# Performance work log

Measured on AMD Instinct MI355X. Metric: run time of the kernel, lower is better.

The kernel has to match this reference:

```python
import jax, jax.numpy as jnp
import numpy as np
import math

D = 128      # out_dim (= d)
H = 4        # n_heads
DK = D // H  # d_k = 32
M = 5        # fixed num types in forward
NN = 15      # fixed N in forward
SQRT_DK = math.sqrt(DK)


def setup_inputs() -> dict:
    key = jax.random.key(0)
    ks = jax.random.split(key, 18)
    b, n = 1024, 64
    inp = {
        "node_inp": jax.random.normal(ks[0], (D, b, n), jnp.float32),
        "WW": jax.random.normal(ks[1], (b, M, n, NN), jnp.float32) * 0.1,
        "mask_matrix": jax.random.uniform(ks[2], (M * NN, n), jnp.float32),
        "R": jax.random.normal(ks[3], (b, H, n, n), jnp.float32),
        "attn_mask": jax.random.uniform(ks[4], (1, 1, n, 4 * n), jnp.float32),
        # learned parameters (xavier-ish scale)
        "WK": jax.random.normal(ks[5], (M, D, D), jnp.float32) * 0.05,
        "bK": jax.random.normal(ks[6], (M, D, 1), jnp.float32) * 0.05,
        "WQ": jax.random.normal(ks[7], (M, D, D), jnp.float32) * 0.05,
        "bQ": jax.random.normal(ks[8], (M, D, 1), jnp.float32) * 0.05,
        "WM": jax.random.normal(ks[9], (M, D, D), jnp.float32) * 0.05,
        "bM": jax.random.normal(ks[10], (M, D, 1), jnp.float32) * 0.05,
        "WB": jax.random.normal(ks[11], (M, D, D), jnp.float32) * 0.05,
        "bB": jax.random.normal(ks[12], (M, D, 1), jnp.float32) * 0.05,
        "Wmsgup": jax.random.normal(ks[13], (DK, DK), jnp.float32) * 0.1,
        "Wmsgdown": jax.random.normal(ks[14], (DK, DK), jnp.float32) * 0.1,
        "Wmsgleft": jax.random.normal(ks[15], (DK, DK), jnp.float32) * 0.1,
        "Wmsgright": jax.random.normal(ks[16], (DK, DK), jnp.float32) * 0.1,
    }
    return inp


def reference(node_inp, WW, mask_matrix, R, attn_mask,
              WK, bK, WQ, bQ, WM, bM, WB, bB,
              Wmsgup, Wmsgdown, Wmsgleft, Wmsgright):
    d, b, n = node_inp.shape
    # project node features through per-type mixing: (b, m, d, N)
    node_inp_m = jnp.einsum('dbn,bmnN->bmdN', node_inp, WW)

    def proj_perm(W, bias):
        # per-type linear then permute(0,2,1,3) before flatten (as K/Q do)
        x = jnp.einsum('mde,bmeN->bmdN', W, node_inp_m) + bias[None]  # (b,m,d,N)
        x = x.transpose(0, 2, 1, 3).reshape(b, d, M * NN)
        return x @ mask_matrix  # (b, d, n)

    K = proj_perm(WK, bK).reshape(b, H, DK, n)
    Q = proj_perm(WQ, bQ).reshape(b, H, DK, n)

    # message: NOTE original reshapes (b*m,d,N) -> (b,d,m*N) WITHOUT the permute; replicate faithfully
    msg = jnp.einsum('mde,bmeN->bmdN', WM, node_inp_m) + bM[None]  # (b,m,d,N)
    message = msg.reshape(b, d, M * NN) @ mask_matrix               # (b, d, n)

    A = jnp.einsum('bhki,bhkj->bhij', Q, K) / SQRT_DK               # (b,h,n,n)
    aw = jax.nn.softmax(R + A, axis=3)
    aw = jnp.where(jnp.isnan(aw), jnp.zeros_like(aw), aw)
    aw = jnp.tile(aw, (1, 1, 1, 4)) * attn_mask                     # (b,h,n,4n)

    res_msg = message.reshape(b, H, DK, n)
    Wmsg = jnp.concatenate([Wmsgup, Wmsgdown, Wmsgleft, Wmsgright], axis=1)  # (dk, 4dk)
    res = jnp.einsum('kq,bhkn->bhqn', Wmsg, res_msg)                # (b,h,4dk,n)
    res = res.reshape(b, H, DK, 4 * n)                               # faithful reshape

    B = jnp.einsum('bhnm,bhkm->bhkn', aw, res).reshape(b, d, n)
    B = jax.nn.gelu(B, approximate=False)

    Bm = jnp.einsum('bdn,bmnN->bmdN', B, WW)
    Bm = jnp.einsum('mde,bmeN->bmdN', WB, Bm) + bB[None]
    Bm = Bm.transpose(0, 2, 1, 3).reshape(b, d, M * NN) @ mask_matrix  # (b,d,n)
    out = Bm.transpose(1, 0, 2) + node_inp                             # (d,b,n)
    return (out, aw[0, 0])
```

## Files before the change

### kernel.cpp

```cpp
#include <hip/hip_runtime.h>
#include <math.h>

#define Dd 128
#define Hh 4
#define DKk 32
#define Mm 5
#define NNn 15
#define Bb 1024
#define Nn 64
#define MN 75
#define BN 65536
#define RSQRT_DK 0.17677669529663687f

typedef __attribute__((ext_vector_type(8))) short bf16x8;
typedef __attribute__((ext_vector_type(4))) float f32x4;

__device__ __forceinline__ ushort f2bf(float x) {
    unsigned u = __float_as_uint(x);
    u = (u + 0x7fffu + ((u >> 16) & 1u)) >> 16;
    return (ushort)u;
}
__device__ __forceinline__ float bf2f(ushort h) {
    return __uint_as_float(((unsigned)h) << 16);
}
__device__ __forceinline__ void split2(float x, ushort& hi, ushort& lo) {
    hi = f2bf(x);
    lo = f2bf(x - bf2f(hi));
}
__device__ __forceinline__ f32x4 MFMA(bf16x8 a, bf16x8 b, f32x4 c) {
    return __builtin_amdgcn_mfma_f32_16x16x32_bf16(a, b, c, 0, 0, 0);
}

#define NSWZ(r, c) ((r) * 128 + ((c) ^ (((r) & 7) << 3)))

__global__ void k0_prep(const float* __restrict__ maskm,
                        const float* __restrict__ WK, const float* __restrict__ bK,
                        const float* __restrict__ WQ, const float* __restrict__ bQ,
                        const float* __restrict__ WM, const float* __restrict__ bM,
                        const float* __restrict__ WB, const float* __restrict__ bB,
                        const float* __restrict__ Wu, const float* __restrict__ Wd,
                        const float* __restrict__ Wl, const float* __restrict__ Wr,
                        ushort* __restrict__ WKhi, ushort* __restrict__ WKlo,
                        ushort* __restrict__ WQhi, ushort* __restrict__ WQlo,
                        ushort* __restrict__ WMhi, ushort* __restrict__ WBhi,
                        ushort* __restrict__ maskhi, ushort* __restrict__ masklo,
                        ushort* __restrict__ maskThi, ushort* __restrict__ maskTlo,
                        float* __restrict__ btKT, float* __restrict__ btQT,
                        float* __restrict__ btMT, float* __restrict__ btB,
                        ushort* __restrict__ WcatT)
{
    int tid = blockIdx.x * blockDim.x + threadIdx.x;
    int nthr = gridDim.x * blockDim.x;
    const int NW = Mm * Dd * Dd;
    for (int i = tid; i < NW; i += nthr) {
        split2(WK[i], WKhi[i], WKlo[i]);
        split2(WQ[i], WQhi[i], WQlo[i]);
        WMhi[i] = f2bf(WM[i]);
        WBhi[i] = f2bf(WB[i]);
    }
    for (int i = tid; i < 96 * 64; i += nthr) {
        float v = (i < MN * 64) ? maskm[i] : 0.f;
        split2(v, maskhi[i], masklo[i]);
    }
    for (int i = tid; i < 64 * 96; i += nthr) {
        int col = i / 96, j = i - col * 96;
        float v = (j < MN) ? maskm[j * 64 + col] : 0.f;
        split2(v, maskThi[i], maskTlo[i]);
    }
    for (int i = tid; i < 4096; i += nthr) {
        int q = i >> 5, kk = i & 31;
        const float* Wsel = (q < 32) ? Wu : (q < 64) ? Wd : (q < 96) ? Wl : Wr;
        WcatT[i] = f2bf(Wsel[kk * 32 + (q & 31)]);
    }
    for (int i = tid; i < 8192; i += nthr) {
        int d = i >> 6, col = i & 63;
        float aKv = 0.f, aQv = 0.f, aBv = 0.f;
        for (int m = 0; m < Mm; ++m) {
            float mrs = 0.f;
            for (int N = 0; N < NNn; ++N) mrs += maskm[(m * 15 + N) * 64 + col];
            aKv += bK[m * 128 + d] * mrs;
            aQv += bQ[m * 128 + d] * mrs;
            aBv += bB[m * 128 + d] * mrs;
        }
        btKT[col * 128 + d] = aKv;
        btQT[col * 128 + d] = aQv;
        btB[i] = aBv;
        float aMv = 0.f;
        for (int j = 0; j < MN; ++j) {
            int f = d * 75 + j;
            int m = f / 1920;
            int dloc = (f / 15) & 127;
            aMv += bM[m * 128 + dloc] * maskm[j * 64 + col];
        }
        btMT[col * 128 + d] = aMv;
    }
}

__global__ __launch_bounds__(512, 6) void k1_proj(
    const float* __restrict__ node, const float* __restrict__ WW,
    const ushort* __restrict__ WKhi, const ushort* __restrict__ WKlo,
    const ushort* __restrict__ WQhi, const ushort* __restrict__ WQlo,
    const ushort* __restrict__ WMhi,
    const ushort* __restrict__ maskThi, const ushort* __restrict__ maskTlo,
    const float* __restrict__ btKT, const float* __restrict__ btQT,
    const float* __restrict__ btMT,
    ushort* __restrict__ Khi, ushort* __restrict__ Klo,
    ushort* __restrict__ Qhi, ushort* __restrict__ Qlo,
    ushort* __restrict__ msgTg)
{
    const int b = blockIdx.x;
    const int tid = threadIdx.x;
    const int lane = tid & 63, w = tid >> 6;
    const int l15 = lane & 15, lq = lane >> 4;

    __shared__ ushort nimTh[80 * 128];
    __shared__ ushort nimTl[80 * 128];
    __shared__ ushort Yh[32 * 104];
    __shared__ ushort Yl[32 * 104];
    ushort* xM = nimTl;

    const f32x4 zz = {0.f, 0.f, 0.f, 0.f};

    for (int t = tid; t < 5 * 128; t += 512) {
        int mm = t >> 7, e = t & 127;
        nimTh[(mm * 16 + 15) * 128 + e] = 0;
        nimTl[(mm * 16 + 15) * 128 + e] = 0;
    }
    for (int t = tid; t < 32 * 29; t += 512) {
        int r = t / 29, cc = 75 + (t - r * 29);
        Yh[r * 104 + cc] = 0;
        Yl[r * 104 + cc] = 0;
    }

    {
        bf16x8 ah[2], al[2];
        #pragma unroll
        for (int ks = 0; ks < 2; ++ks) {
            const float* np = node + (size_t)(w * 16 + l15) * BN + b * 64 + ks * 32 + lq * 8;
            float tmp[8];
            *(float4*)tmp       = *(const float4*)np;
            *(float4*)(tmp + 4) = *(const float4*)(np + 4);
            #pragma unroll
            for (int j = 0; j < 8; ++j) {
                ushort h_, l_; split2(tmp[j], h_, l_);
                ah[ks][j] = (short)h_; al[ks][j] = (short)l_;
            }
        }
        for (int m = 0; m < Mm; ++m) {
            const float* wp = WW + ((size_t)b * Mm + m) * 960 + (l15 < 15 ? l15 : 0);
            f32x4 chh = zz, chl = zz, clh = zz;
            #pragma unroll
            for (int ks = 0; ks < 2; ++ks) {
                bf16x8 bh, bl;
                #pragma unroll
                for (int t = 0; t < 8; ++t) {
                    int n = ks * 32 + lq * 8 + t;
                    float v = (l15 < 15) ? wp[n * 15] : 0.f;
                    ushort h_, l_; split2(v, h_, l_);
                    bh[t] = (short)h_; bl[t] = (short)l_;
                }
                chh = MFMA(ah[ks], bh, chh);
                chl = MFMA(ah[ks], bl, chl);
                clh = MFMA(al[ks], bh, clh);
            }
            f32x4 c = chh + chl + clh;
            if (l15 < 15) {
                int row = m * 16 + l15;
                #pragma unroll
                for (int t = 0; t < 4; ++t) {
                    int e = w * 16 + lq * 4 + t;
                    split2(c[t], nimTh[NSWZ(row, e)], nimTl[NSWZ(row, e)]);
                }
            }
        }
    }
    __syncthreads();

    for (int P = 0; P < 2; ++P) {
        const ushort* Whi = P ? WQhi : WKhi;
        const ushort* Wlo = P ? WQlo : WKlo;
        const float*  btP = P ? btQT : btKT;
        ushort* Phi = P ? Qhi : Khi;
        ushort* Plo = P ? Qlo : Klo;

        for (int qd = 0; qd < 4; ++qd) {
            for (int u = w; u < 10; u += 8) {
                int m = u >> 1, rt = u & 1;
                int d0 = qd * 32 + rt * 16 + l15;
                f32x4 phh = zz, phl = zz, plh = zz;
                #pragma unroll
                for (int ks = 0; ks < 4; ++ks) {
                    int k0 = ks * 32 + lq * 8;
                    size_t wo = (size_t)m * 16384 + (size_t)d0 * 128 + k0;
                    bf16x8 awh = *(const bf16x8*)(Whi + wo);
                    bf16x8 awl = *(const bf16x8*)(Wlo + wo);
                    int nrow = m * 16 + l15;
                    bf16x8 bh = *(const bf16x8*)(&nimTh[NSWZ(nrow, k0)]);
                    bf16x8 bl = *(const bf16x8*)(&nimTl[NSWZ(nrow, k0)]);
                    phh = MFMA(awh, bh, phh); phl = MFMA(awh, bl, phl); plh = MFMA(awl, bh, plh);
                }
                f32x4 c = phh + phl + plh;
                if (l15 < 15) {
                    int j = m * 15 + l15;
                    #pragma unroll
                    for (int t = 0; t < 4; ++t) {
                        int r = rt * 16 + lq * 4 + t;
                        split2(c[t], Yh[r * 104 + j], Yl[r * 104 + j]);
                    }
                }
            }
            __syncthreads();
            {
                int nr = w & 3, dc = w >> 2;
                f32x4 phh = zz, phl = zz, plh = zz;
                #pragma unroll
                for (int ks = 0; ks < 3; ++ks) {
                    int k0 = ks * 32 + lq * 8;
                    bf16x8 mh = *(const bf16x8*)(maskThi + (nr * 16 + l15) * 96 + k0);
                    bf16x8 ml = *(const bf16x8*)(maskTlo + (nr * 16 + l15) * 96 + k0);
                    bf16x8 yh = *(const bf16x8*)(&Yh[(dc * 16 + l15) * 104 + k0]);
                    bf16x8 yl = *(const bf16x8*)(&Yl[(dc * 16 + l15) * 104 + k0]);
                    phh = MFMA(mh, yh, phh); phl = MFMA(ml, yh, phl); plh = MFMA(mh, yl, plh);
                }
                f32x4 c = phh + phl + plh;
                #pragma unroll
                for (int t = 0; t < 4; ++t) {
                    int n = nr * 16 + lq * 4 + t;
                    int dloc = dc * 16 + l15;
                    int d = qd * 32 + dloc;
                    size_t oi = (((size_t)(b * 4 + qd)) * 64 + n) * 32 + dloc;
                    ushort hh_, ll_;
                    split2(c[t] + btP[n * 128 + d], hh_, ll_);
                    Phi[oi] = hh_; Plo[oi] = ll_;
                }
            }
            __syncthreads();
        }
    }

    for (int t = tid; t < 128 * 5; t += 512) {
        int r = t / 5, cc = 75 + (t - r * 5);
        xM[r * 80 + cc] = 0;
    }
    {
        int rt = w;
        for (int m = 0; m < Mm; ++m) {
            f32x4 c0 = zz, c1 = zz;
            #pragma unroll
            for (int ks = 0; ks < 4; ++ks) {
                int k0 = ks * 32 + lq * 8;
                bf16x8 a  = *(const bf16x8*)(WMhi + (size_t)m * 16384 + (size_t)(rt * 16 + l15) * 128 + k0);
                int nrow = m * 16 + l15;
                bf16x8 bh = *(const bf16x8*)(&nimTh[NSWZ(nrow, k0)]);
                if (ks < 2) c0 = MFMA(a, bh, c0); else c1 = MFMA(a, bh, c1);
            }
            f32x4 c = c0 + c1;
            if (l15 < 15) {
                #pragma unroll
                for (int t = 0; t < 4; ++t) {
                    int dflat = rt * 16 + lq * 4 + t;
                    int g = m * 1920 + dflat * 15 + l15;
                    xM[(g / 75) * 80 + (g % 75)] = f2bf(c[t]);
                }
            }
        }
    }
    __syncthreads();
    #pragma unroll
    for (int s = 0; s < 4; ++s) {
        int u = w * 4 + s;
        int nr = u & 3, ddc = u >> 2;
        f32x4 cs0 = zz, cs1 = zz, cs2 = zz;
        {
            bf16x8 a0 = *(const bf16x8*)(maskThi + (nr * 16 + l15) * 96 + lq * 8);
            bf16x8 b0 = *(const bf16x8*)(&xM[(ddc * 16 + l15) * 80 + lq * 8]);
            cs0 = MFMA(a0, b0, cs0);
            bf16x8 a1 = *(const bf16x8*)(maskThi + (nr * 16 + l15) * 96 + 32 + lq * 8);
            bf16x8 b1 = *(const bf16x8*)(&xM[(ddc * 16 + l15) * 80 + 32 + lq * 8]);
            cs1 = MFMA(a1, b1, cs1);
            bf16x8 a2 = *(const bf16x8*)(maskThi + (nr * 16 + l15) * 96 + 64 + lq * 8);
            bf16x8 b2 = *(const bf16x8*)(&xM[(ddc * 16 + l15) * 80 + 64 + lq * 8]);
            cs2 = MFMA(a2, b2, cs2);
        }
        f32x4 c = cs0 + cs1 + cs2;
        #pragma unroll
        for (int t = 0; t < 4; ++t) {
            int n = nr * 16 + lq * 4 + t;
            int dd = ddc * 16 + l15;
            int h = dd >> 5, dk = dd & 31;
            msgTg[(((size_t)(b * 4 + h)) * 64 + n) * 32 + dk] = f2bf(c[t] + btMT[n * 128 + dd]);
        }
    }
}

__global__ __launch_bounds__(512, 4) void k2_attn(
    const ushort* __restrict__ Khi, const ushort* __restrict__ Klo,
    const ushort* Qhi, const ushort* __restrict__ Qlo,
    const ushort* __restrict__ msgTg,
    const float* __restrict__ R, const float* __restrict__ am,
    const ushort* __restrict__ WcatT, float* __restrict__ aw00,
    ushort* Bout)
{
    const int b = blockIdx.x >> 2, h = blockIdx.x & 3;
    const int tid = threadIdx.x;
    const int lane = tid & 63, w = tid >> 6;
    const int l15 = lane & 15, lq = lane >> 4;

    __shared__ float  ST[64 * 65];
    __shared__ ushort resS[128 * 72];
    __shared__ ushort awq[64 * 72];

    const f32x4 zz = {0.f, 0.f, 0.f, 0.f};
    const size_t base2 = (size_t)(b * 4 + h) * 2048;
    const float* Rb = R + (size_t)(b * 4 + h) * 4096;

    {
        int ti = w >> 1;
        bf16x8 ah = *(const bf16x8*)(Qhi + base2 + (size_t)(ti * 16 + l15) * 32 + lq * 8);
        bf16x8 al = *(const bf16x8*)(Qlo + base2 + (size_t)(ti * 16 + l15) * 32 + lq * 8);
        #pragma unroll
        for (int s = 0; s < 2; ++s) {
            int tj = (w & 1) * 2 + s;
            bf16x8 bh = *(const bf16x8*)(Khi + base2 + (size_t)(tj * 16 + l15) * 32 + lq * 8);
            bf16x8 bl = *(const bf16x8*)(Klo + base2 + (size_t)(tj * 16 + l15) * 32 + lq * 8);
            f32x4 chh = zz, chl = zz, clh = zz;
            chh = MFMA(ah, bh, chh); chl = MFMA(ah, bl, chl); clh = MFMA(al, bh, clh);
            f32x4 c = chh + chl + clh;
            #pragma unroll
            for (int r = 0; r < 4; ++r) {
                int i = ti * 16 + lq * 4 + r, j = tj * 16 + l15;
                ST[j * 65 + i] = Rb[i * 64 + j] + c[r] * RSQRT_DK;
            }
        }
    }
    {
        bf16x8 a = *(const bf16x8*)(WcatT + (w * 16 + l15) * 32 + lq * 8);
        #pragma unroll
        for (int nt = 0; nt < 4; ++nt) {
            bf16x8 bfr = *(const bf16x8*)(msgTg + base2 + (size_t)(nt * 16 + l15) * 32 + lq * 8);
            f32x4 c = MFMA(a, bfr, zz);
            #pragma unroll
            for (int r = 0; r < 4; ++r)
                resS[(w * 16 + lq * 4 + r) * 72 + nt * 16 + l15] = f2bf(c[r]);
        }
    }
    __syncthreads();

    {
        int row = tid >> 3, part = tid & 7;
        float v[8]; float mx = -INFINITY;
        #pragma unroll
        for (int jj = 0; jj < 8; ++jj) { v[jj] = ST[(part * 8 + jj) * 65 + row]; mx = fmaxf(mx, v[jj]); }
        mx = fmaxf(mx, __shfl_xor(mx, 1));
        mx = fmaxf(mx, __shfl_xor(mx, 2));
        mx = fmaxf(mx, __shfl_xor(mx, 4));
        float s = 0.f;
        #pragma unroll
        for (int jj = 0; jj < 8; ++jj) { v[jj] = expf(v[jj] - mx); s += v[jj]; }
        s += __shfl_xor(s, 1); s += __shfl_xor(s, 2); s += __shfl_xor(s, 4);
        float inv = 1.f / s;
        #pragma unroll
        for (int jj = 0; jj < 8; ++jj) {
            float p = v[jj] * inv;
            ST[(part * 8 + jj) * 65 + row] = isnan(p) ? 0.f : p;
        }
    }
    __syncthreads();

    const int kt = w >> 2, it = w & 3;
    f32x4 accB0 = zz, accB1 = zz;
    for (int q = 0; q < 4; ++q) {
        for (int e = tid; e < 4096; e += 512) {
            int i = e >> 6, j0 = e & 63;
            float p = ST[j0 * 65 + i] * am[i * 256 + q * 64 + j0];
            awq[i * 72 + j0] = f2bf(p);
            if (blockIdx.x == 0) aw00[i * 256 + q * 64 + j0] = p;
        }
        __syncthreads();
        int row = 4 * (kt * 16 + l15) + q;
        bf16x8 a0 = *(const bf16x8*)(&resS[row * 72 + lq * 8]);
        bf16x8 b0 = *(const bf16x8*)(&awq[(it * 16 + l15) * 72 + lq * 8]);
        accB0 = MFMA(a0, b0, accB0);
        bf16x8 a1 = *(const bf16x8*)(&resS[row * 72 + 32 + lq * 8]);
        bf16x8 b1 = *(const bf16x8*)(&awq[(it * 16 + l15) * 72 + 32 + lq * 8]);
        accB1 = MFMA(a1, b1, accB1);
        __syncthreads();
    }
    f32x4 accB = accB0 + accB1;

    #pragma unroll
    for (int r = 0; r < 4; ++r) {
        int k = kt * 16 + lq * 4 + r, i = it * 16 + l15;
        float x = accB[r];
        float g = 0.5f * x * (1.f + erff(x * 0.70710678118654752f));
        Bout[base2 + k * 64 + i] = f2bf(g);
    }
}

__global__ __launch_bounds__(512, 4) void k3_out(
    const ushort* Bbuf, const float* __restrict__ WW,
    const ushort* __restrict__ WBhi, const ushort* __restrict__ maskhi,
    const float* __restrict__ btB, const float* __restrict__ node,
    float* __restrict__ outp)
{
    const int b = blockIdx.x, tid = threadIdx.x;
    const int lane = tid & 63, w = tid >> 6, l15 = lane & 15, lq = lane >> 4;
    __shared__ ushort sB[128 * 72];
    __shared__ ushort wwh[64 * 17];
    __shared__ ushort t1[128 * 17];
    __shared__ ushort nm[32 * 66];

    for (int i = tid; i < 8192; i += 512) {
        int d = i >> 6, n = i & 63;
        sB[d * 72 + n] = Bbuf[(size_t)b * 8192 + i];
    }
    const f32x4 zz = {0.f, 0.f, 0.f, 0.f};
    f32x4 acc[4];
    for (int c = 0; c < 4; ++c) acc[c] = zz;
    __syncthreads();

    for (int m = 0; m < Mm; ++m) {
        for (int i = tid; i < 64 * 17; i += 512) {
            int n = i / 17, N = i - n * 17;
            wwh[i] = (N < 15) ? f2bf(WW[(((size_t)b * Mm + m) * 64 + n) * 15 + N]) : (ushort)0;
        }
        __syncthreads();
        {
            f32x4 c0 = zz, c1 = zz;
            #pragma unroll
            for (int ks = 0; ks < 2; ++ks) {
                int k0 = ks * 32 + (lq << 3);
                bf16x8 a = *(const bf16x8*)(&sB[(w * 16 + l15) * 72 + k0]);
                bf16x8 bh;
                #pragma unroll
                for (int t = 0; t < 8; ++t) bh[t] = (short)wwh[(k0 + t) * 17 + l15];
                if (ks == 0) c0 = MFMA(a, bh, c0); else c1 = MFMA(a, bh, c1);
            }
            f32x4 c = c0 + c1;
            #pragma unroll
            for (int t = 0; t < 4; ++t)
                t1[(w * 16 + lq * 4 + t) * 17 + l15] = f2bf(c[t]);
        }
        __syncthreads();

        bf16x8 mfh;
        {
            int ct = w & 3;
            int k0 = lq << 3;
            #pragma unroll
            for (int t = 0; t < 8; ++t) {
                int kk = k0 + t;
                int row = (kk < 15) ? (m * 15 + kk) : 95;
                mfh[t] = (short)maskhi[row * 64 + ct * 16 + l15];
            }
        }
        for (int eb = 0; eb < 4; ++eb) {
            {
                int rtl = w >> 2, ct = w & 3;
                int e = eb * 32 + rtl * 16 + l15;
                int k0 = lq << 3;
                bf16x8 a;
                #pragma unroll
                for (int t = 0; t < 8; ++t) {
                    int kk = k0 + t;
                    int cc = (kk < 15) ? kk : 15;
                    a[t] = (short)t1[e * 17 + cc];
                }
                f32x4 c = zz;
                c = MFMA(a, mfh, c);
                #pragma unroll
                for (int t = 0; t < 4; ++t)
                    nm[(rtl * 16 + lq * 4 + t) * 66 + ct * 16 + l15] = f2bf(c[t]);
            }
            __syncthreads();
            {
                size_t aoff = (size_t)(w * 16 + l15) * 128 + eb * 32 + (lq << 3);
                bf16x8 a = *(const bf16x8*)(WBhi + m * 16384 + aoff);
                int k0 = lq << 3;
                #pragma unroll
                for (int ct = 0; ct < 4; ++ct) {
                    bf16x8 bh;
                    #pragma unroll
                    for (int t = 0; t < 8; ++t) bh[t] = (short)nm[(k0 + t) * 66 + ct * 16 + l15];
                    acc[ct] = MFMA(a, bh, acc[ct]);
                }
            }
            __syncthreads();
        }
    }
    #pragma unroll
    for (int ct = 0; ct < 4; ++ct) {
        #pragma unroll
        for (int t = 0; t < 4; ++t) {
            int d = w * 16 + lq * 4 + t;
            int col = ct * 16 + l15;
            size_t gi = (size_t)d * BN + b * 64 + col;
            outp[gi] = acc[ct][t] + btB[d * 64 + col] + node[gi];
        }
    }
}

extern "C" void kernel_launch(void* const* d_in, const int* in_sizes, int n_in,
                              void* d_out, int out_size, void* d_ws, size_t ws_size,
                              hipStream_t stream) {
    const float* node  = (const float*)d_in[0];
    const float* WW    = (const float*)d_in[1];
    const float* maskm = (const float*)d_in[2];
    const float* R     = (const float*)d_in[3];
    const float* am    = (const float*)d_in[4];
    const float* WK = (const float*)d_in[5];  const float* bK = (const float*)d_in[6];
    const float* WQ = (const float*)d_in[7];  const float* bQ = (const float*)d_in[8];
    const float* WM = (const float*)d_in[9];  const float* bM = (const float*)d_in[10];
    const float* WB = (const float*)d_in[11]; const float* bB = (const float*)d_in[12];
    const float* Wu = (const float*)d_in[13]; const float* Wd = (const float*)d_in[14];
    const float* Wl = (const float*)d_in[15]; const float* Wr = (const float*)d_in[16];

    float* out  = (float*)d_out;
    float* aw00 = out + (size_t)Dd * BN;

    ushort* Khi = (ushort*)d_out;
    ushort* Klo = Khi + 8388608;

    char* W = (char*)d_ws;
    ushort* Qhi   = (ushort*)W;
    ushort* Qlo   = Qhi + 8388608;
    ushort* msgTg = Qlo + 8388608;
    ushort* WKhi  = msgTg + 8388608;
    ushort* WKlo  = WKhi + 81920;
    ushort* WQhi  = WKlo + 81920;
    ushort* WQlo  = WQhi + 81920;
    ushort* WMhi  = WQlo + 81920;
    ushort* WBhi  = WMhi + 81920;
    ushort* maskhi  = WBhi + 81920;
    ushort* masklo  = maskhi + 6144;
    ushort* maskThi = masklo + 6144;
    ushort* maskTlo = maskThi + 6144;
    ushort* WcatT   = maskTlo + 6144;
    float*  btKT = (float*)(WcatT + 4096);
    float*  btQT = btKT + 8192;
    float*  btMT = btQT + 8192;
    float*  btB  = btMT + 8192;

    k0_prep<<<512, 256, 0, stream>>>(maskm, WK, bK, WQ, bQ, WM, bM, WB, bB,
                                     Wu, Wd, Wl, Wr,
                                     WKhi, WKlo, WQhi, WQlo, WMhi, WBhi,
                                     maskhi, masklo, maskThi, maskTlo,
                                     btKT, btQT, btMT, btB, WcatT);
    k1_proj<<<Bb, 512, 0, stream>>>(node, WW, WKhi, WKlo, WQhi, WQlo, WMhi,
                                    maskThi, maskTlo, btKT, btQT, btMT,
                                    Khi, Klo, Qhi, Qlo, msgTg);
    k2_attn<<<Bb * Hh, 512, 0, stream>>>(Khi, Klo, Qhi, Qlo, msgTg, R, am,
                                         WcatT, aw00, Qhi );
    k3_out<<<Bb, 512, 0, stream>>>(Qhi , WW, WBhi, maskhi, btB, node, out);
}
```

Baseline: 319.2 us.

## Restructure k1 K/Q projection to keep intermediates in registers via shuffles

The K/Q projection in k1 now computes the per-type linear output in registers and moves it into the mask-matmul B operand with wave shuffles. This removes the shared-memory Y staging buffers and the per-quarter __syncthreads. A new padded 80-column transposed mask layout is prepared in k0 to match the register layout. k1 also drops from 512 to 256 threads per block with more work per wave, which lowers LDS use and the barrier count, but increases register pressure and adds many shuffle instructions.

```diff
diff --git a/kernel.cpp b/kernel.cpp
--- a/kernel.cpp
+++ b/kernel.cpp
@@ -29,6 +29,11 @@
 }
 __device__ __forceinline__ f32x4 MFMA(bf16x8 a, bf16x8 b, f32x4 c) {
     return __builtin_amdgcn_mfma_f32_16x16x32_bf16(a, b, c, 0, 0, 0);
+}
+__device__ __forceinline__ bf16x8 mk8(unsigned u0, unsigned u1, unsigned u2, unsigned u3) {
+    union { unsigned u[4]; bf16x8 v; } x;
+    x.u[0] = u0; x.u[1] = u1; x.u[2] = u2; x.u[3] = u3;
+    return x.v;
 }
 
 #define NSWZ(r, c) ((r) * 128 + ((c) ^ (((r) & 7) << 3)))
@@ -45,6 +50,7 @@
                         ushort* __restrict__ WMhi, ushort* __restrict__ WBhi,
                         ushort* __restrict__ maskhi, ushort* __restrict__ masklo,
                         ushort* __restrict__ maskThi, ushort* __restrict__ maskTlo,
+                        ushort* __restrict__ maskT80hi, ushort* __restrict__ maskT80lo,
                         float* __restrict__ btKT, float* __restrict__ btQT,
                         float* __restrict__ btMT, float* __restrict__ btB,
                         ushort* __restrict__ WcatT)
@@ -67,6 +73,12 @@
         float v = (j < MN) ? maskm[j * 64 + col] : 0.f;
         split2(v, maskThi[i], maskTlo[i]);
     }
+    for (int i = tid; i < 64 * 96; i += nthr) {
+        int col = i / 96, jt = i - col * 96;
+        int m = jt >> 4, jj = jt & 15;
+        float v = (jt < 80 && jj < 15) ? maskm[(m * 15 + jj) * 64 + col] : 0.f;
+        split2(v, maskT80hi[i], maskT80lo[i]);
+    }
     for (int i = tid; i < 4096; i += nthr) {
         int q = i >> 5, kk = i & 31;
         const float* Wsel = (q < 32) ? Wu : (q < 64) ? Wd : (q < 96) ? Wl : Wr;
@@ -96,12 +108,13 @@
     }
 }
 
-__global__ __launch_bounds__(512, 6) void k1_proj(
+__global__ __launch_bounds__(256, 4) void k1_proj(
     const float* __restrict__ node, const float* __restrict__ WW,
     const ushort* __restrict__ WKhi, const ushort* __restrict__ WKlo,
     const ushort* __restrict__ WQhi, const ushort* __restrict__ WQlo,
     const ushort* __restrict__ WMhi,
-    const ushort* __restrict__ maskThi, const ushort* __restrict__ maskTlo,
+    const ushort* __restrict__ maskThi,
+    const ushort* __restrict__ maskT80hi, const ushort* __restrict__ maskT80lo,
     const float* __restrict__ btKT, const float* __restrict__ btQT,
     const float* __restrict__ btMT,
     ushort* __restrict__ Khi, ushort* __restrict__ Klo,
@@ -112,31 +125,20 @@
     const int tid = threadIdx.x;
     const int lane = tid & 63, w = tid >> 6;
     const int l15 = lane & 15, lq = lane >> 4;
-
-    __shared__ ushort nimTh[80 * 128];
-    __shared__ ushort nimTl[80 * 128];
-    __shared__ ushort Yh[32 * 104];
-    __shared__ ushort Yl[32 * 104];
+    const int lcl = (l15 < 15) ? l15 : 14;
+
+    __shared__ __align__(16) ushort nimTh[79 * 128];
+    __shared__ __align__(16) ushort nimTl[80 * 128 + 16];
     ushort* xM = nimTl;
 
     const f32x4 zz = {0.f, 0.f, 0.f, 0.f};
 
-    for (int t = tid; t < 5 * 128; t += 512) {
-        int mm = t >> 7, e = t & 127;
-        nimTh[(mm * 16 + 15) * 128 + e] = 0;
-        nimTl[(mm * 16 + 15) * 128 + e] = 0;
-    }
-    for (int t = tid; t < 32 * 29; t += 512) {
-        int r = t / 29, cc = 75 + (t - r * 29);
-        Yh[r * 104 + cc] = 0;
-        Yl[r * 104 + cc] = 0;
-    }
-
-    {
+    for (int s = 0; s < 2; ++s) {
+        int eb = w * 2 + s;
         bf16x8 ah[2], al[2];
         #pragma unroll
         for (int ks = 0; ks < 2; ++ks) {
-            const float* np = node + (size_t)(w * 16 + l15) * BN + b * 64 + ks * 32 + lq * 8;
+            const float* np = node + (size_t)(eb * 16 + l15) * BN + b * 64 + ks * 32 + lq * 8;
             float tmp[8];
             *(float4*)tmp       = *(const float4*)np;
             *(float4*)(tmp + 4) = *(const float4*)(np + 4);
@@ -168,13 +170,17 @@
                 int row = m * 16 + l15;
                 #pragma unroll
                 for (int t = 0; t < 4; ++t) {
-                    int e = w * 16 + lq * 4 + t;
+                    int e = eb * 16 + lq * 4 + t;
                     split2(c[t], nimTh[NSWZ(row, e)], nimTl[NSWZ(row, e)]);
                 }
             }
         }
     }
     __syncthreads();
+
+    const int sAl = ((lq & 1) << 5) + l15;
+    const int sBl = sAl + 16;
+    const bool hiT = (lq >= 2);
 
     for (int P = 0; P < 2; ++P) {
         const ushort* Whi = P ? WQhi : WKhi;
@@ -182,76 +188,107 @@
         const float*  btP = P ? btQT : btKT;
         ushort* Phi = P ? Qhi : Khi;
         ushort* Plo = P ? Qlo : Klo;
-
-        for (int qd = 0; qd < 4; ++qd) {
-            for (int u = w; u < 10; u += 8) {
-                int m = u >> 1, rt = u & 1;
-                int d0 = qd * 32 + rt * 16 + l15;
-                f32x4 phh = zz, phl = zz, plh = zz;
+        const int dct = w;
+
+        for (int dt = 0; dt < 2; ++dt) {
+            unsigned pkh0[5], pkh1[5], pkl0[5], pkl1[5];
+            #pragma unroll
+            for (int m = 0; m < Mm; ++m) {
+                int arow = m * 16 + lcl;
+                int wrow = dct * 32 + dt * 16 + l15;
+                f32x4 chh = zz, chl = zz, clh = zz;
                 #pragma unroll
                 for (int ks = 0; ks < 4; ++ks) {
                     int k0 = ks * 32 + lq * 8;
-                    size_t wo = (size_t)m * 16384 + (size_t)d0 * 128 + k0;
-                    bf16x8 awh = *(const bf16x8*)(Whi + wo);
-                    bf16x8 awl = *(const bf16x8*)(Wlo + wo);
-                    int nrow = m * 16 + l15;
-                    bf16x8 bh = *(const bf16x8*)(&nimTh[NSWZ(nrow, k0)]);
-                    bf16x8 bl = *(const bf16x8*)(&nimTl[NSWZ(nrow, k0)]);
-                    phh = MFMA(awh, bh, phh); phl = MFMA(awh, bl, phl); plh = MFMA(awl, bh, plh);
-                }
-                f32x4 c = phh + phl + plh;
-                if (l15 < 15) {
-                    int j = m * 15 + l15;
-                    #pragma unroll
-                    for (int t = 0; t < 4; ++t) {
-                        int r = rt * 16 + lq * 4 + t;
-                        split2(c[t], Yh[r * 104 + j], Yl[r * 104 + j]);
-                    }
-                }
-            }
-            __syncthreads();
-            {
-                int nr = w & 3, dc = w >> 2;
-                f32x4 phh = zz, phl = zz, plh = zz;
-                #pragma unroll
-                for (int ks = 0; ks < 3; ++ks) {
-                    int k0 = ks * 32 + lq * 8;
-                    bf16x8 mh = *(const bf16x8*)(maskThi + (nr * 16 + l15) * 96 + k0);
-                    bf16x8 ml = *(const bf16x8*)(maskTlo + (nr * 16 + l15) * 96 + k0);
-                    bf16x8 yh = *(const bf16x8*)(&Yh[(dc * 16 + l15) * 104 + k0]);
-                    bf16x8 yl = *(const bf16x8*)(&Yl[(dc * 16 + l15) * 104 + k0]);
-                    phh = MFMA(mh, yh, phh); phl = MFMA(ml, yh, phl); plh = MFMA(mh, yl, plh);
-                }
-                f32x4 c = phh + phl + plh;
-                #pragma unroll
-                for (int t = 0; t < 4; ++t) {
-                    int n = nr * 16 + lq * 4 + t;
-                    int dloc = dc * 16 + l15;
-                    int d = qd * 32 + dloc;
-                    size_t oi = (((size_t)(b * 4 + qd)) * 64 + n) * 32 + dloc;
+                    bf16x8 anh = *(const bf16x8*)&nimTh[NSWZ(arow, k0)];
+                    bf16x8 anl = *(const bf16x8*)&nimTl[NSWZ(arow, k0)];
+                    size_t wo = (size_t)m * 16384 + (size_t)wrow * 128 + k0;
+                    bf16x8 bwh = *(const bf16x8*)(Whi + wo);
+                    bf16x8 bwl = *(const bf16x8*)(Wlo + wo);
+                    chh = MFMA(anh, bwh, chh);
+                    chl = MFMA(anh, bwl, chl);
+                    clh = MFMA(anl, bwh, clh);
+                }
+                f32x4 c = chh + chl + clh;
+                ushort h0, h1, h2, h3, l0, l1, l2, l3;
+                split2(c[0], h0, l0); split2(c[1], h1, l1);
+                split2(c[2], h2, l2); split2(c[3], h3, l3);
+                pkh0[m] = (unsigned)h0 | ((unsigned)h1 << 16);
+                pkh1[m] = (unsigned)h2 | ((unsigned)h3 << 16);
+                pkl0[m] = (unsigned)l0 | ((unsigned)l1 << 16);
+                pkl1[m] = (unsigned)l2 | ((unsigned)l3 << 16);
+            }
+            f32x4 aH[4] = {zz, zz, zz, zz};
+            f32x4 aX[4] = {zz, zz, zz, zz};
+            #pragma unroll
+            for (int ks = 0; ks < 3; ++ks) {
+                const int mA = ks * 2;
+                const int mB = (ks * 2 + 1 < 5) ? ks * 2 + 1 : 4;
+                unsigned a0, b0c;
+                bf16x8 yH, yL;
+                {
+                    unsigned u0, u1, u2, u3;
+                    a0 = __shfl((int)pkh0[mA], sAl); b0c = __shfl((int)pkh0[mB], sAl);
+                    u0 = hiT ? b0c : a0;
+                    a0 = __shfl((int)pkh1[mA], sAl); b0c = __shfl((int)pkh1[mB], sAl);
+                    u1 = hiT ? b0c : a0;
+                    a0 = __shfl((int)pkh0[mA], sBl); b0c = __shfl((int)pkh0[mB], sBl);
+                    u2 = hiT ? b0c : a0;
+                    a0 = __shfl((int)pkh1[mA], sBl); b0c = __shfl((int)pkh1[mB], sBl);
+                    u3 = hiT ? b0c : a0;
+                    yH = mk8(u0, u1, u2, u3);
+                    a0 = __shfl((int)pkl0[mA], sAl); b0c = __shfl((int)pkl0[mB], sAl);
+                    u0 = hiT ? b0c : a0;
+                    a0 = __shfl((int)pkl1[mA], sAl); b0c = __shfl((int)pkl1[mB], sAl);
+                    u1 = hiT ? b0c : a0;
+                    a0 = __shfl((int)pkl0[mA], sBl); b0c = __shfl((int)pkl0[mB], sBl);
+                    u2 = hiT ? b0c : a0;
+                    a0 = __shfl((int)pkl1[mA], sBl); b0c = __shfl((int)pkl1[mB], sBl);
+                    u3 = hiT ? b0c : a0;
+                    yL = mk8(u0, u1, u2, u3);
+                }
+                #pragma unroll
+                for (int nt = 0; nt < 4; ++nt) {
+                    int mr = (nt * 16 + l15) * 96 + ks * 32 + lq * 8;
+                    bf16x8 mh = *(const bf16x8*)(maskT80hi + mr);
+                    bf16x8 ml = *(const bf16x8*)(maskT80lo + mr);
+                    aH[nt] = MFMA(mh, yH, aH[nt]);
+                    aX[nt] = MFMA(ml, yH, aX[nt]);
+                    aX[nt] = MFMA(mh, yL, aX[nt]);
+                }
+            }
+            #pragma unroll
+            for (int nt = 0; nt < 4; ++nt) {
+                f32x4 c = aH[nt] + aX[nt];
+                #pragma unroll
+                for (int r = 0; r < 4; ++r) {
+                    int n = nt * 16 + lq * 4 + r;
+                    int dpr = dct * 32 + dt * 16 + l15;
+                    size_t oi = (((size_t)(b * 4 + dct)) * 64 + n) * 32 + dt * 16 + l15;
                     ushort hh_, ll_;
-                    split2(c[t] + btP[n * 128 + d], hh_, ll_);
+                    split2(c[r] + btP[n * 128 + dpr], hh_, ll_);
                     Phi[oi] = hh_; Plo[oi] = ll_;
                 }
             }
-            __syncthreads();
-        }
-    }
-
-    for (int t = tid; t < 128 * 5; t += 512) {
+        }
+    }
+    __syncthreads();
+
+    for (int t = tid; t < 128 * 5; t += 256) {
         int r = t / 5, cc = 75 + (t - r * 5);
         xM[r * 80 + cc] = 0;
     }
-    {
-        int rt = w;
+    for (int t = tid; t < 16; t += 256) xM[10240 + t] = 0;
+    for (int s = 0; s < 2; ++s) {
+        int rt = w * 2 + s;
         for (int m = 0; m < Mm; ++m) {
             f32x4 c0 = zz, c1 = zz;
+            int arow = m * 16 + lcl;
             #pragma unroll
             for (int ks = 0; ks < 4; ++ks) {
                 int k0 = ks * 32 + lq * 8;
                 bf16x8 a  = *(const bf16x8*)(WMhi + (size_t)m * 16384 + (size_t)(rt * 16 + l15) * 128 + k0);
-                int nrow = m * 16 + l15;
-                bf16x8 bh = *(const bf16x8*)(&nimTh[NSWZ(nrow, k0)]);
+                bf16x8 bh = *(const bf16x8*)&nimTh[NSWZ(arow, k0)];
                 if (ks < 2) c0 = MFMA(a, bh, c0); else c1 = MFMA(a, bh, c1);
             }
             f32x4 c = c0 + c1;
@@ -266,9 +303,10 @@
         }
     }
     __syncthreads();
+
     #pragma unroll
-    for (int s = 0; s < 4; ++s) {
-        int u = w * 4 + s;
+    for (int s2 = 0; s2 < 8; ++s2) {
+        int u = w * 8 + s2;
         int nr = u & 3, ddc = u >> 2;
         f32x4 cs0 = zz, cs1 = zz, cs2 = zz;
         {
@@ -535,7 +573,9 @@
     ushort* masklo  = maskhi + 6144;
     ushort* maskThi = masklo + 6144;
     ushort* maskTlo = maskThi + 6144;
-    ushort* WcatT   = maskTlo + 6144;
+    ushort* maskT80hi = maskTlo + 6144;
+    ushort* maskT80lo = maskT80hi + 6144;
+    ushort* WcatT   = maskT80lo + 6144;
     float*  btKT = (float*)(WcatT + 4096);
     float*  btQT = btKT + 8192;
     float*  btMT = btQT + 8192;
@@ -545,9 +585,11 @@
                                      Wu, Wd, Wl, Wr,
                                      WKhi, WKlo, WQhi, WQlo, WMhi, WBhi,
                                      maskhi, masklo, maskThi, maskTlo,
+                                     maskT80hi, maskT80lo,
                                      btKT, btQT, btMT, btB, WcatT);
-    k1_proj<<<Bb, 512, 0, stream>>>(node, WW, WKhi, WKlo, WQhi, WQlo, WMhi,
-                                    maskThi, maskTlo, btKT, btQT, btMT,
+    k1_proj<<<Bb, 256, 0, stream>>>(node, WW, WKhi, WKlo, WQhi, WQlo, WMhi,
+                                    maskThi, maskT80hi, maskT80lo,
+                                    btKT, btQT, btMT,
                                     Khi, Klo, Qhi, Qlo, msgTg);
     k2_attn<<<Bb * Hh, 512, 0, stream>>>(Khi, Klo, Qhi, Qlo, msgTg, R, am,
                                          WcatT, aw00, Qhi );
```

Measured after the change: 566.8 us. 77.6% more time.
